# Optimization experiments

Measured on AMD Instinct MI355X. Metric: run time of the kernel, lower is better.

## Reference

```python
import jax, jax.numpy as jnp
import numpy as np

SEQ, BATCH, HIDDEN, HEADS = 2048, 2, 1024, 16
HEAD_DIM = HIDDEN // HEADS
NORM = float(np.sqrt(HEAD_DIM))
NEG_MIN = float(np.finfo(np.float32).min)


def setup_inputs() -> dict:
    key = jax.random.key(0)
    ks = jax.random.split(key, 9)
    xavier = lambda k: (jax.random.normal(k, (HIDDEN, HIDDEN), jnp.float32)
                        * np.sqrt(2.0 / (HIDDEN + HIDDEN)))
    hidden_states = jax.random.normal(ks[0], (SEQ, BATCH, HIDDEN), jnp.float32)
    # causal (left-to-right) bool mask, True = attend
    attention_mask = jnp.tril(jnp.ones((SEQ, SEQ), dtype=bool))[None, None, :, :]
    return {
        "hidden_states": hidden_states,
        "attention_mask": attention_mask,
        "Wq": xavier(ks[1]), "bq": jnp.zeros((HIDDEN,), jnp.float32),
        "Wk": xavier(ks[2]), "bk": jnp.zeros((HIDDEN,), jnp.float32),
        "Wv": xavier(ks[3]), "bv": jnp.zeros((HIDDEN,), jnp.float32),
        "Wo": xavier(ks[4]), "bo": jnp.zeros((HIDDEN,), jnp.float32),
    }


def reference(hidden_states, attention_mask, Wq, bq, Wk, bk, Wv, bv, Wo, bo):
    s, b, _ = hidden_states.shape
    # projections (F.linear: x @ W.T + b), seq-first layout -> [s,b,h,d]
    q = (hidden_states @ Wq.T + bq).reshape(s, b, HEADS, HEAD_DIM) / NORM
    k = (hidden_states @ Wk.T + bk).reshape(s, b, HEADS, HEAD_DIM)
    v = (hidden_states @ Wv.T + bv).reshape(s, b, HEADS, HEAD_DIM)
    # scores [b,h,q,k] (Q already pre-scaled by 1/sqrt(d))
    scores = jnp.einsum("qbhd,kbhd->bhqk", q, k)
    scores = jnp.where(attention_mask, scores, NEG_MIN)
    probs = jax.nn.softmax(scores, axis=-1)
    # context [b,h,q,d] -> permute(2,0,1,3) -> [q,b,h,d] -> [q,b,hidden]
    ctx = jnp.einsum("bhqk,kbhd->qbhd", probs, v).reshape(s, b, HIDDEN)
    return ctx @ Wo.T + bo
```

## Files before the change

### kernel.cpp

```cpp
#include <hip/hip_runtime.h>
#include <hip/hip_bf16.h>
#include <cstdint>
#include <math.h>

#define SEQ 2048
#define BATCH 2
#define HID 1024
#define NH 16
#define HD 64
#define MROWS (SEQ * BATCH)

typedef __attribute__((ext_vector_type(8))) short bf16x8;
typedef __attribute__((ext_vector_type(4))) float f32x4;

typedef const __attribute__((address_space(1))) void* gas_t;
typedef __attribute__((address_space(3))) void* las_t;

static __device__ __forceinline__ unsigned short f2bf(float x) {
    __hip_bfloat16 h = __float2bfloat16(x);
    unsigned short u;
    __builtin_memcpy(&u, &h, 2);
    return u;
}

__global__ __launch_bounds__(256) void f2bf_kern(const float* __restrict__ in,
                                                 unsigned short* __restrict__ out,
                                                 int n8) {
    int i = blockIdx.x * 256 + threadIdx.x;
    if (i >= n8) return;
    const float4* p = (const float4*)in + (size_t)i * 2;
    float4 a = p[0], b = p[1];
    union { unsigned short us[8]; uint4 v; } o;
    o.us[0] = f2bf(a.x); o.us[1] = f2bf(a.y); o.us[2] = f2bf(a.z); o.us[3] = f2bf(a.w);
    o.us[4] = f2bf(b.x); o.us[5] = f2bf(b.y); o.us[6] = f2bf(b.z); o.us[7] = f2bf(b.w);
    ((uint4*)out)[i] = o.v;
}

#define GBK 32

__global__ __launch_bounds__(256, 4) void gemm_bf16(
    const unsigned short* __restrict__ A, const unsigned short* __restrict__ W,
    const float* __restrict__ b0, const float* __restrict__ b1,
    const float* __restrict__ b2,
    unsigned short* __restrict__ Qo, unsigned short* __restrict__ Ko,
    unsigned short* __restrict__ Vo, float* __restrict__ Fo, int mode) {
    __shared__ unsigned short As[2][64 * GBK];
    __shared__ unsigned short Bs[2][128 * GBK];
    const int t = threadIdx.x;
    const int lane = t & 63, w = t >> 6;
    const int wr = w & 1, wc = w >> 1;
    const int m0 = blockIdx.x * 64, n0 = blockIdx.y * 128;

    f32x4 acc[2][4];
#pragma unroll
    for (int i = 0; i < 2; ++i)
#pragma unroll
        for (int j = 0; j < 4; ++j) acc[i][j] = {0.f, 0.f, 0.f, 0.f};

    const int srow = w * 16 + (lane >> 2);
    const int scol = (lane & 3) * 8;
    const unsigned short* gA = A + (size_t)(m0 + srow) * HID + scol;
    const unsigned short* gB = W + (size_t)(n0 + srow) * HID + scol;

    auto stage = [&](int buf, int k0) {
        __builtin_amdgcn_global_load_lds((gas_t)(gA + k0),
                                         (las_t)(&As[buf][(w * 16) * GBK]), 16, 0, 0);
#pragma unroll
        for (int c = 0; c < 2; ++c)
            __builtin_amdgcn_global_load_lds((gas_t)(gB + (size_t)c * 64 * HID + k0),
                                             (las_t)(&Bs[buf][(c * 64 + w * 16) * GBK]), 16, 0, 0);
    };

    const int arow = wr * 32 + (lane & 15);
    const int brow = wc * 64 + (lane & 15);
    const int kfo = (lane >> 4) * 8;

    stage(0, 0);
    int cur = 0;
    for (int k0 = 0; k0 < HID; k0 += GBK) {
        __syncthreads();
        if (k0 + GBK < HID) stage(cur ^ 1, k0 + GBK);
        bf16x8 af[2], bfr[4];
#pragma unroll
        for (int mt = 0; mt < 2; ++mt)
            af[mt] = *(const bf16x8*)(&As[cur][(arow + mt * 16) * GBK + kfo]);
#pragma unroll
        for (int nt = 0; nt < 4; ++nt)
            bfr[nt] = *(const bf16x8*)(&Bs[cur][(brow + nt * 16) * GBK + kfo]);
#pragma unroll
        for (int mt = 0; mt < 2; ++mt)
#pragma unroll
            for (int nt = 0; nt < 4; ++nt)
                acc[mt][nt] = __builtin_amdgcn_mfma_f32_16x16x32_bf16(
                    af[mt], bfr[nt], acc[mt][nt], 0, 0, 0);
        cur ^= 1;
    }

    const int seg = n0 >> 10;
    const float* bias = (mode == 1) ? b0 : (seg == 0 ? b0 : (seg == 1 ? b1 : b2));
    const float scale = (mode == 0 && seg == 0) ? 0.125f : 1.0f;
    const int nbase = (n0 & 1023) + wc * 64;

    float bvals[4];
#pragma unroll
    for (int nt = 0; nt < 4; ++nt)
        bvals[nt] = bias[nbase + nt * 16 + (lane & 15)];

#pragma unroll
    for (int mt = 0; mt < 2; ++mt)
#pragma unroll
        for (int nt = 0; nt < 4; ++nt)
#pragma unroll
            for (int i = 0; i < 4; ++i) {
                float v = (acc[mt][nt][i] + bvals[nt]) * scale;
                int m = m0 + wr * 32 + mt * 16 + (lane >> 4) * 4 + i;
                int n = nbase + nt * 16 + (lane & 15);
                if (mode == 1) {
                    Fo[(size_t)m * HID + n] = v;
                } else if (seg == 0) {
                    Qo[(size_t)m * HID + n] = f2bf(v);
                } else if (seg == 1) {
                    Ko[(size_t)m * HID + n] = f2bf(v);
                } else {
                    Vo[(size_t)n * MROWS + (m & 1) * SEQ + (m >> 1)] = f2bf(v);
                }
            }
}

__global__ __launch_bounds__(256) void attn_mfma(const unsigned short* __restrict__ Qb,
                                                 const unsigned short* __restrict__ Kb,
                                                 const unsigned short* __restrict__ Vt,
                                                 unsigned short* __restrict__ Ob) {
    __shared__ unsigned short Kl[2][64 * 64];
    __shared__ unsigned short Vl[2][64 * 64];
    __shared__ unsigned short QP[64 * 64];

    const int t = threadIdx.x;
    const int lane = t & 63, w = t >> 6;

    const int flat = (int)blockIdx.x + (int)blockIdx.y * 16;
    const int xcd = flat & 7, ii = flat >> 3;
    const int bh = xcd * 4 + (ii >> 4);
    const int p = ii & 15;
    const int b = bh >> 4, h = bh & 15;

    const int lrow_base = w * 8 + (lane >> 3);
    const int chunkb = (lane & 7) * 16;

    for (int pass = 0; pass < 2; ++pass) {
        const int qt = pass == 0 ? (31 - p) : p;
        const int q0 = qt * 64;
        if (pass) __syncthreads();

        auto stage_kv = [&](int buf, int kt) {
            const int k0 = kt * 64;
#pragma unroll
            for (int c = 0; c < 2; ++c) {
                int lr = c * 32 + lrow_base;
                int sb = chunkb ^ ((lr & 7) << 4);
                const unsigned short* ksrc =
                    Kb + ((size_t)(k0 + lr) * 2 + b) * HID + h * 64 + (sb >> 1);
                const unsigned short* vsrc =
                    Vt + (size_t)(h * 64 + lr) * MROWS + b * SEQ + k0 + (sb >> 1);
                __builtin_amdgcn_global_load_lds((gas_t)ksrc,
                    (las_t)(&Kl[buf][(c * 32 + w * 8) * 64]), 16, 0, 0);
                __builtin_amdgcn_global_load_lds((gas_t)vsrc,
                    (las_t)(&Vl[buf][(c * 32 + w * 8) * 64]), 16, 0, 0);
            }
        };

        stage_kv(0, 0);

#pragma unroll
        for (int c = 0; c < 2; ++c) {
            int f = c * 256 + t;
            int r = f >> 3, dc = f & 7;
            uint4 v = *(const uint4*)(Qb + (size_t)((q0 + r) * 2 + b) * HID + h * 64 + dc * 8);
            *(uint4*)((char*)QP + r * 128 + ((dc * 16) ^ ((r & 7) << 4))) = v;
        }

        f32x4 acc[4];
#pragma unroll
        for (int nt = 0; nt < 4; ++nt) acc[nt] = {0.f, 0.f, 0.f, 0.f};
        float mrow[4] = {-INFINITY, -INFINITY, -INFINITY, -INFINITY};
        float lrow[4] = {0.f, 0.f, 0.f, 0.f};
        bf16x8 qf[2];

        int cur = 0;
        for (int kt = 0; kt <= qt; ++kt) {
            __syncthreads();
            if (kt < qt) stage_kv(cur ^ 1, kt + 1);
            if (kt == 0) {
                int r = w * 16 + (lane & 15);
                int base = r * 128, sw = (r & 7) << 4;
                qf[0] = *(const bf16x8*)((char*)QP + base + ((((lane >> 4) * 16) + 0) ^ sw));
                qf[1] = *(const bf16x8*)((char*)QP + base + ((((lane >> 4) * 16) + 64) ^ sw));
            }
            const char* Kc = (const char*)Kl[cur];
            const char* Vc = (const char*)Vl[cur];

            f32x4 s[4];
#pragma unroll
            for (int ct = 0; ct < 4; ++ct) {
                int j = ct * 16 + (lane & 15);
                int base = j * 128, sw = (j & 7) << 4;
                bf16x8 kf0 = *(const bf16x8*)(Kc + base + ((((lane >> 4) * 16) + 0) ^ sw));
                bf16x8 kf1 = *(const bf16x8*)(Kc + base + ((((lane >> 4) * 16) + 64) ^ sw));
                f32x4 z = {0.f, 0.f, 0.f, 0.f};
                z = __builtin_amdgcn_mfma_f32_16x16x32_bf16(qf[0], kf0, z, 0, 0, 0);
                z = __builtin_amdgcn_mfma_f32_16x16x32_bf16(qf[1], kf1, z, 0, 0, 0);
                s[ct] = z;
            }

            if (kt == qt) {
#pragma unroll
                for (int ct = 0; ct < 4; ++ct) {
                    int j = ct * 16 + (lane & 15);
#pragma unroll
                    for (int i = 0; i < 4; ++i) {
                        int q = w * 16 + (lane >> 4) * 4 + i;
                        if (j > q) s[ct][i] = -3.0e38f;
                    }
                }
            }

#pragma unroll
            for (int i = 0; i < 4; ++i) {
                float mx = fmaxf(fmaxf(s[0][i], s[1][i]), fmaxf(s[2][i], s[3][i]));
                mx = fmaxf(mx, __shfl_xor(mx, 1));
                mx = fmaxf(mx, __shfl_xor(mx, 2));
                mx = fmaxf(mx, __shfl_xor(mx, 4));
                mx = fmaxf(mx, __shfl_xor(mx, 8));
                float mn = fmaxf(mrow[i], mx);
                float corr = __expf(mrow[i] - mn);
                mrow[i] = mn;
                float rs = 0.f;
#pragma unroll
                for (int ct = 0; ct < 4; ++ct) {
                    float pe = __expf(s[ct][i] - mn);
                    s[ct][i] = pe;
                    rs += pe;
                }
                rs += __shfl_xor(rs, 1);
                rs += __shfl_xor(rs, 2);
                rs += __shfl_xor(rs, 4);
                rs += __shfl_xor(rs, 8);
                lrow[i] = lrow[i] * corr + rs;
#pragma unroll
                for (int nt = 0; nt < 4; ++nt) acc[nt][i] *= corr;
            }

#pragma unroll
            for (int ct = 0; ct < 4; ++ct)
#pragma unroll
                for (int i = 0; i < 4; ++i) {
                    int r = w * 16 + (lane >> 4) * 4 + i;
                    int jb = (ct * 16 + (lane & 15)) * 2;
                    *(unsigned short*)((char*)QP + r * 128 + (jb ^ ((r & 7) << 4))) = f2bf(s[ct][i]);
                }
            asm volatile("s_waitcnt lgkmcnt(0)" ::: "memory");
            __builtin_amdgcn_sched_barrier(0);

            bf16x8 pf[2];
            {
                int r = w * 16 + (lane & 15);
                int base = r * 128, sw = (r & 7) << 4;
                pf[0] = *(const bf16x8*)((char*)QP + base + ((((lane >> 4) * 16) + 0) ^ sw));
                pf[1] = *(const bf16x8*)((char*)QP + base + ((((lane >> 4) * 16) + 64) ^ sw));
            }
#pragma unroll
            for (int nt = 0; nt < 4; ++nt) {
                int d = nt * 16 + (lane & 15);
                int base = d * 128, sw = (d & 7) << 4;
                bf16x8 v0 = *(const bf16x8*)(Vc + base + ((((lane >> 4) * 16) + 0) ^ sw));
                bf16x8 v1 = *(const bf16x8*)(Vc + base + ((((lane >> 4) * 16) + 64) ^ sw));
                acc[nt] = __builtin_amdgcn_mfma_f32_16x16x32_bf16(pf[0], v0, acc[nt], 0, 0, 0);
                acc[nt] = __builtin_amdgcn_mfma_f32_16x16x32_bf16(pf[1], v1, acc[nt], 0, 0, 0);
            }
            cur ^= 1;
        }

#pragma unroll
        for (int i = 0; i < 4; ++i) {
            float inv = 1.0f / lrow[i];
            int q = q0 + w * 16 + (lane >> 4) * 4 + i;
#pragma unroll
            for (int nt = 0; nt < 4; ++nt) {
                int col = h * 64 + nt * 16 + (lane & 15);
                Ob[(size_t)(q * 2 + b) * HID + col] = f2bf(acc[nt][i] * inv);
            }
        }
    }
}

extern "C" void kernel_launch(void* const* d_in, const int* in_sizes, int n_in,
                              void* d_out, int out_size, void* d_ws, size_t ws_size,
                              hipStream_t stream) {
    const float* hs = (const float*)d_in[0];
    const float* Wq = (const float*)d_in[2];
    const float* bq = (const float*)d_in[3];
    const float* Wk = (const float*)d_in[4];
    const float* bk = (const float*)d_in[5];
    const float* Wv = (const float*)d_in[6];
    const float* bv = (const float*)d_in[7];
    const float* Wo = (const float*)d_in[8];
    const float* bo = (const float*)d_in[9];

    char* ws = (char*)d_ws;
    unsigned short* hs_bf   = (unsigned short*)(ws);
    unsigned short* Wqkv_bf = (unsigned short*)(ws + (8u << 20));
    unsigned short* Wo_bf   = (unsigned short*)(ws + (14u << 20));
    unsigned short* Q_bf    = (unsigned short*)(ws + (16u << 20));
    unsigned short* K_bf    = (unsigned short*)(ws + (24u << 20));
    unsigned short* Vt_bf   = (unsigned short*)(ws + (32u << 20));
    unsigned short* ctx_bf  = (unsigned short*)(ws + (40u << 20));

    dim3 blk(256);
    const int WN8 = HID * HID / 8;
    hipLaunchKernelGGL(f2bf_kern, dim3(MROWS * HID / 8 / 256), blk, 0, stream, hs, hs_bf, MROWS * HID / 8);
    hipLaunchKernelGGL(f2bf_kern, dim3(WN8 / 256), blk, 0, stream, Wq, Wqkv_bf, WN8);
    hipLaunchKernelGGL(f2bf_kern, dim3(WN8 / 256), blk, 0, stream, Wk, Wqkv_bf + (size_t)HID * HID, WN8);
    hipLaunchKernelGGL(f2bf_kern, dim3(WN8 / 256), blk, 0, stream, Wv, Wqkv_bf + (size_t)2 * HID * HID, WN8);
    hipLaunchKernelGGL(f2bf_kern, dim3(WN8 / 256), blk, 0, stream, Wo, Wo_bf, WN8);

    hipLaunchKernelGGL(gemm_bf16, dim3(MROWS / 64, 24), blk, 0, stream,
                       hs_bf, Wqkv_bf, bq, bk, bv, Q_bf, K_bf, Vt_bf, (float*)nullptr, 0);

    hipLaunchKernelGGL(attn_mfma, dim3(16, 32), blk, 0, stream,
                       Q_bf, K_bf, Vt_bf, ctx_bf);

    hipLaunchKernelGGL(gemm_bf16, dim3(MROWS / 64, 8), blk, 0, stream,
                       ctx_bf, Wo_bf, bo, bo, bo,
                       (unsigned short*)nullptr, (unsigned short*)nullptr,
                       (unsigned short*)nullptr, (float*)d_out, 1);
}
```

Measured before the change: 245.7 us.

## Enlarge GEMM tiles via template and give each attention block one query tile

The GEMM becomes a template with 128-row M tiles and a variable N tile: 128 columns for the QKV projection and 64 for the output projection. This raises register reuse per block while keeping the output-projection grid large enough. The attention kernel no longer pairs a long and a short query tile in two passes. It launches one block per query tile (32x32 grid), longest tiles first, spreading causal work across more blocks at the cost of losing the explicit load pairing. The GEMM also drops its occupancy hint of 4 blocks, which may change register allocation.

```diff
diff --git a/kernel.cpp b/kernel.cpp
--- a/kernel.cpp
+++ b/kernel.cpp
@@ -38,41 +38,43 @@
 
 #define GBK 32
 
-__global__ __launch_bounds__(256, 4) void gemm_bf16(
+template <int BNT2>
+__global__ __launch_bounds__(256) void gemm_bf16(
     const unsigned short* __restrict__ A, const unsigned short* __restrict__ W,
     const float* __restrict__ b0, const float* __restrict__ b1,
     const float* __restrict__ b2,
     unsigned short* __restrict__ Qo, unsigned short* __restrict__ Ko,
     unsigned short* __restrict__ Vo, float* __restrict__ Fo, int mode) {
-    __shared__ unsigned short As[2][64 * GBK];
-    __shared__ unsigned short Bs[2][128 * GBK];
+    constexpr int BN = BNT2 * 32;
+    __shared__ unsigned short As[2][128 * GBK];
+    __shared__ unsigned short Bs[2][BN * GBK];
     const int t = threadIdx.x;
     const int lane = t & 63, w = t >> 6;
     const int wr = w & 1, wc = w >> 1;
-    const int m0 = blockIdx.x * 64, n0 = blockIdx.y * 128;
-
-    f32x4 acc[2][4];
-#pragma unroll
-    for (int i = 0; i < 2; ++i)
-#pragma unroll
-        for (int j = 0; j < 4; ++j) acc[i][j] = {0.f, 0.f, 0.f, 0.f};
-
-    const int srow = w * 16 + (lane >> 2);
-    const int scol = (lane & 3) * 8;
-    const unsigned short* gA = A + (size_t)(m0 + srow) * HID + scol;
-    const unsigned short* gB = W + (size_t)(n0 + srow) * HID + scol;
+    const int m0 = blockIdx.x * 128, n0 = blockIdx.y * BN;
+
+    f32x4 acc[4][BNT2];
+#pragma unroll
+    for (int i = 0; i < 4; ++i)
+#pragma unroll
+        for (int j = 0; j < BNT2; ++j) acc[i][j] = {0.f, 0.f, 0.f, 0.f};
+
+    const unsigned short* gA = A + (size_t)(m0 + w * 16 + (lane >> 2)) * HID + (lane & 3) * 8;
+    const unsigned short* gB = W + (size_t)(n0 + w * 16 + (lane >> 2)) * HID + (lane & 3) * 8;
 
     auto stage = [&](int buf, int k0) {
-        __builtin_amdgcn_global_load_lds((gas_t)(gA + k0),
-                                         (las_t)(&As[buf][(w * 16) * GBK]), 16, 0, 0);
 #pragma unroll
         for (int c = 0; c < 2; ++c)
+            __builtin_amdgcn_global_load_lds((gas_t)(gA + (size_t)c * 64 * HID + k0),
+                                             (las_t)(&As[buf][(c * 64 + w * 16) * GBK]), 16, 0, 0);
+#pragma unroll
+        for (int c = 0; c < BN / 64; ++c)
             __builtin_amdgcn_global_load_lds((gas_t)(gB + (size_t)c * 64 * HID + k0),
                                              (las_t)(&Bs[buf][(c * 64 + w * 16) * GBK]), 16, 0, 0);
     };
 
-    const int arow = wr * 32 + (lane & 15);
-    const int brow = wc * 64 + (lane & 15);
+    const int arow = wr * 64 + (lane & 15);
+    const int brow = wc * (BNT2 * 16) + (lane & 15);
     const int kfo = (lane >> 4) * 8;
 
     stage(0, 0);
@@ -80,17 +82,17 @@
     for (int k0 = 0; k0 < HID; k0 += GBK) {
         __syncthreads();
         if (k0 + GBK < HID) stage(cur ^ 1, k0 + GBK);
-        bf16x8 af[2], bfr[4];
-#pragma unroll
-        for (int mt = 0; mt < 2; ++mt)
+        bf16x8 af[4], bfr[BNT2];
+#pragma unroll
+        for (int mt = 0; mt < 4; ++mt)
             af[mt] = *(const bf16x8*)(&As[cur][(arow + mt * 16) * GBK + kfo]);
 #pragma unroll
-        for (int nt = 0; nt < 4; ++nt)
+        for (int nt = 0; nt < BNT2; ++nt)
             bfr[nt] = *(const bf16x8*)(&Bs[cur][(brow + nt * 16) * GBK + kfo]);
 #pragma unroll
-        for (int mt = 0; mt < 2; ++mt)
-#pragma unroll
-            for (int nt = 0; nt < 4; ++nt)
+        for (int mt = 0; mt < 4; ++mt)
+#pragma unroll
+            for (int nt = 0; nt < BNT2; ++nt)
                 acc[mt][nt] = __builtin_amdgcn_mfma_f32_16x16x32_bf16(
                     af[mt], bfr[nt], acc[mt][nt], 0, 0, 0);
         cur ^= 1;
@@ -99,21 +101,21 @@
     const int seg = n0 >> 10;
     const float* bias = (mode == 1) ? b0 : (seg == 0 ? b0 : (seg == 1 ? b1 : b2));
     const float scale = (mode == 0 && seg == 0) ? 0.125f : 1.0f;
-    const int nbase = (n0 & 1023) + wc * 64;
-
-    float bvals[4];
-#pragma unroll
-    for (int nt = 0; nt < 4; ++nt)
+    const int nbase = (n0 & 1023) + wc * (BNT2 * 16);
+
+    float bvals[BNT2];
+#pragma unroll
+    for (int nt = 0; nt < BNT2; ++nt)
         bvals[nt] = bias[nbase + nt * 16 + (lane & 15)];
 
 #pragma unroll
-    for (int mt = 0; mt < 2; ++mt)
-#pragma unroll
-        for (int nt = 0; nt < 4; ++nt)
+    for (int mt = 0; mt < 4; ++mt)
+#pragma unroll
+        for (int nt = 0; nt < BNT2; ++nt)
 #pragma unroll
             for (int i = 0; i < 4; ++i) {
                 float v = (acc[mt][nt][i] + bvals[nt]) * scale;
-                int m = m0 + wr * 32 + mt * 16 + (lane >> 4) * 4 + i;
+                int m = m0 + wr * 64 + mt * 16 + (lane >> 4) * 4 + i;
                 int n = nbase + nt * 16 + (lane & 15);
                 if (mode == 1) {
                     Fo[(size_t)m * HID + n] = v;
@@ -138,157 +140,152 @@
     const int t = threadIdx.x;
     const int lane = t & 63, w = t >> 6;
 
-    const int flat = (int)blockIdx.x + (int)blockIdx.y * 16;
+    const int flat = (int)blockIdx.x + (int)blockIdx.y * 32;
     const int xcd = flat & 7, ii = flat >> 3;
-    const int bh = xcd * 4 + (ii >> 4);
-    const int p = ii & 15;
+    const int bh = xcd * 4 + (ii >> 5);
+    const int qt = 31 - (ii & 31);
     const int b = bh >> 4, h = bh & 15;
+    const int q0 = qt * 64;
 
     const int lrow_base = w * 8 + (lane >> 3);
     const int chunkb = (lane & 7) * 16;
 
-    for (int pass = 0; pass < 2; ++pass) {
-        const int qt = pass == 0 ? (31 - p) : p;
-        const int q0 = qt * 64;
-        if (pass) __syncthreads();
-
-        auto stage_kv = [&](int buf, int kt) {
-            const int k0 = kt * 64;
-#pragma unroll
-            for (int c = 0; c < 2; ++c) {
-                int lr = c * 32 + lrow_base;
-                int sb = chunkb ^ ((lr & 7) << 4);
-                const unsigned short* ksrc =
-                    Kb + ((size_t)(k0 + lr) * 2 + b) * HID + h * 64 + (sb >> 1);
-                const unsigned short* vsrc =
-                    Vt + (size_t)(h * 64 + lr) * MROWS + b * SEQ + k0 + (sb >> 1);
-                __builtin_amdgcn_global_load_lds((gas_t)ksrc,
-                    (las_t)(&Kl[buf][(c * 32 + w * 8) * 64]), 16, 0, 0);
-                __builtin_amdgcn_global_load_lds((gas_t)vsrc,
-                    (las_t)(&Vl[buf][(c * 32 + w * 8) * 64]), 16, 0, 0);
-            }
-        };
-
-        stage_kv(0, 0);
-
+    auto stage_kv = [&](int buf, int kt) {
+        const int k0 = kt * 64;
 #pragma unroll
         for (int c = 0; c < 2; ++c) {
-            int f = c * 256 + t;
-            int r = f >> 3, dc = f & 7;
-            uint4 v = *(const uint4*)(Qb + (size_t)((q0 + r) * 2 + b) * HID + h * 64 + dc * 8);
-            *(uint4*)((char*)QP + r * 128 + ((dc * 16) ^ ((r & 7) << 4))) = v;
-        }
-
-        f32x4 acc[4];
-#pragma unroll
-        for (int nt = 0; nt < 4; ++nt) acc[nt] = {0.f, 0.f, 0.f, 0.f};
-        float mrow[4] = {-INFINITY, -INFINITY, -INFINITY, -INFINITY};
-        float lrow[4] = {0.f, 0.f, 0.f, 0.f};
-        bf16x8 qf[2];
-
-        int cur = 0;
-        for (int kt = 0; kt <= qt; ++kt) {
-            __syncthreads();
-            if (kt < qt) stage_kv(cur ^ 1, kt + 1);
-            if (kt == 0) {
-                int r = w * 16 + (lane & 15);
-                int base = r * 128, sw = (r & 7) << 4;
-                qf[0] = *(const bf16x8*)((char*)QP + base + ((((lane >> 4) * 16) + 0) ^ sw));
-                qf[1] = *(const bf16x8*)((char*)QP + base + ((((lane >> 4) * 16) + 64) ^ sw));
-            }
-            const char* Kc = (const char*)Kl[cur];
-            const char* Vc = (const char*)Vl[cur];
-
-            f32x4 s[4];
+            int lr = c * 32 + lrow_base;
+            int sb = chunkb ^ ((lr & 7) << 4);
+            const unsigned short* ksrc =
+                Kb + ((size_t)(k0 + lr) * 2 + b) * HID + h * 64 + (sb >> 1);
+            const unsigned short* vsrc =
+                Vt + (size_t)(h * 64 + lr) * MROWS + b * SEQ + k0 + (sb >> 1);
+            __builtin_amdgcn_global_load_lds((gas_t)ksrc,
+                (las_t)(&Kl[buf][(c * 32 + w * 8) * 64]), 16, 0, 0);
+            __builtin_amdgcn_global_load_lds((gas_t)vsrc,
+                (las_t)(&Vl[buf][(c * 32 + w * 8) * 64]), 16, 0, 0);
+        }
+    };
+
+    stage_kv(0, 0);
+
+#pragma unroll
+    for (int c = 0; c < 2; ++c) {
+        int f = c * 256 + t;
+        int r = f >> 3, dc = f & 7;
+        uint4 v = *(const uint4*)(Qb + (size_t)((q0 + r) * 2 + b) * HID + h * 64 + dc * 8);
+        *(uint4*)((char*)QP + r * 128 + ((dc * 16) ^ ((r & 7) << 4))) = v;
+    }
+
+    f32x4 acc[4];
+#pragma unroll
+    for (int nt = 0; nt < 4; ++nt) acc[nt] = {0.f, 0.f, 0.f, 0.f};
+    float mrow[4] = {-INFINITY, -INFINITY, -INFINITY, -INFINITY};
+    float lrow[4] = {0.f, 0.f, 0.f, 0.f};
+    bf16x8 qf[2];
+
+    int cur = 0;
+    for (int kt = 0; kt <= qt; ++kt) {
+        __syncthreads();
+        if (kt < qt) stage_kv(cur ^ 1, kt + 1);
+        if (kt == 0) {
+            int r = w * 16 + (lane & 15);
+            int base = r * 128, sw = (r & 7) << 4;
+            qf[0] = *(const bf16x8*)((char*)QP + base + ((((lane >> 4) * 16) + 0) ^ sw));
+            qf[1] = *(const bf16x8*)((char*)QP + base + ((((lane >> 4) * 16) + 64) ^ sw));
+        }
+        const char* Kc = (const char*)Kl[cur];
+        const char* Vc = (const char*)Vl[cur];
+
+        f32x4 s[4];
+#pragma unroll
+        for (int ct = 0; ct < 4; ++ct) {
+            int j = ct * 16 + (lane & 15);
+            int base = j * 128, sw = (j & 7) << 4;
+            bf16x8 kf0 = *(const bf16x8*)(Kc + base + ((((lane >> 4) * 16) + 0) ^ sw));
+            bf16x8 kf1 = *(const bf16x8*)(Kc + base + ((((lane >> 4) * 16) + 64) ^ sw));
+            f32x4 z = {0.f, 0.f, 0.f, 0.f};
+            z = __builtin_amdgcn_mfma_f32_16x16x32_bf16(qf[0], kf0, z, 0, 0, 0);
+            z = __builtin_amdgcn_mfma_f32_16x16x32_bf16(qf[1], kf1, z, 0, 0, 0);
+            s[ct] = z;
+        }
+
+        if (kt == qt) {
 #pragma unroll
             for (int ct = 0; ct < 4; ++ct) {
                 int j = ct * 16 + (lane & 15);
-                int base = j * 128, sw = (j & 7) << 4;
-                bf16x8 kf0 = *(const bf16x8*)(Kc + base + ((((lane >> 4) * 16) + 0) ^ sw));
-                bf16x8 kf1 = *(const bf16x8*)(Kc + base + ((((lane >> 4) * 16) + 64) ^ sw));
-                f32x4 z = {0.f, 0.f, 0.f, 0.f};
-                z = __builtin_amdgcn_mfma_f32_16x16x32_bf16(qf[0], kf0, z, 0, 0, 0);
-                z = __builtin_amdgcn_mfma_f32_16x16x32_bf16(qf[1], kf1, z, 0, 0, 0);
-                s[ct] = z;
-            }
-
-            if (kt == qt) {
-#pragma unroll
-                for (int ct = 0; ct < 4; ++ct) {
-                    int j = ct * 16 + (lane & 15);
-#pragma unroll
-                    for (int i = 0; i < 4; ++i) {
-                        int q = w * 16 + (lane >> 4) * 4 + i;
-                        if (j > q) s[ct][i] = -3.0e38f;
-                    }
+#pragma unroll
+                for (int i = 0; i < 4; ++i) {
+                    int q = w * 16 + (lane >> 4) * 4 + i;
+                    if (j > q) s[ct][i] = -3.0e38f;
                 }
             }
-
+        }
+
+#pragma unroll
+        for (int i = 0; i < 4; ++i) {
+            float mx = fmaxf(fmaxf(s[0][i], s[1][i]), fmaxf(s[2][i], s[3][i]));
+            mx = fmaxf(mx, __shfl_xor(mx, 1));
+            mx = fmaxf(mx, __shfl_xor(mx, 2));
+            mx = fmaxf(mx, __shfl_xor(mx, 4));
+            mx = fmaxf(mx, __shfl_xor(mx, 8));
+            float mn = fmaxf(mrow[i], mx);
+            float corr = __expf(mrow[i] - mn);
+            mrow[i] = mn;
+            float rs = 0.f;
+#pragma unroll
+            for (int ct = 0; ct < 4; ++ct) {
+                float pe = __expf(s[ct][i] - mn);
+                s[ct][i] = pe;
+                rs += pe;
+            }
+            rs += __shfl_xor(rs, 1);
+            rs += __shfl_xor(rs, 2);
+            rs += __shfl_xor(rs, 4);
+            rs += __shfl_xor(rs, 8);
+            lrow[i] = lrow[i] * corr + rs;
+#pragma unroll
+            for (int nt = 0; nt < 4; ++nt) acc[nt][i] *= corr;
+        }
+
+#pragma unroll
+        for (int ct = 0; ct < 4; ++ct)
 #pragma unroll
             for (int i = 0; i < 4; ++i) {
-                float mx = fmaxf(fmaxf(s[0][i], s[1][i]), fmaxf(s[2][i], s[3][i]));
-                mx = fmaxf(mx, __shfl_xor(mx, 1));
-                mx = fmaxf(mx, __shfl_xor(mx, 2));
-                mx = fmaxf(mx, __shfl_xor(mx, 4));
-                mx = fmaxf(mx, __shfl_xor(mx, 8));
-                float mn = fmaxf(mrow[i], mx);
-                float corr = __expf(mrow[i] - mn);
-                mrow[i] = mn;
-                float rs = 0.f;
-#pragma unroll
-                for (int ct = 0; ct < 4; ++ct) {
-                    float pe = __expf(s[ct][i] - mn);
-                    s[ct][i] = pe;
-                    rs += pe;
-                }
-                rs += __shfl_xor(rs, 1);
-                rs += __shfl_xor(rs, 2);
-                rs += __shfl_xor(rs, 4);
-                rs += __shfl_xor(rs, 8);
-                lrow[i] = lrow[i] * corr + rs;
-#pragma unroll
-                for (int nt = 0; nt < 4; ++nt) acc[nt][i] *= corr;
+                int r = w * 16 + (lane >> 4) * 4 + i;
+                int jb = (ct * 16 + (lane & 15)) * 2;
+                *(unsigned short*)((char*)QP + r * 128 + (jb ^ ((r & 7) << 4))) = f2bf(s[ct][i]);
             }
-
-#pragma unroll
-            for (int ct = 0; ct < 4; ++ct)
-#pragma unroll
-                for (int i = 0; i < 4; ++i) {
-                    int r = w * 16 + (lane >> 4) * 4 + i;
-                    int jb = (ct * 16 + (lane & 15)) * 2;
-                    *(unsigned short*)((char*)QP + r * 128 + (jb ^ ((r & 7) << 4))) = f2bf(s[ct][i]);
-                }
-            asm volatile("s_waitcnt lgkmcnt(0)" ::: "memory");
-            __builtin_amdgcn_sched_barrier(0);
-
-            bf16x8 pf[2];
-            {
-                int r = w * 16 + (lane & 15);
-                int base = r * 128, sw = (r & 7) << 4;
-                pf[0] = *(const bf16x8*)((char*)QP + base + ((((lane >> 4) * 16) + 0) ^ sw));
-                pf[1] = *(const bf16x8*)((char*)QP + base + ((((lane >> 4) * 16) + 64) ^ sw));
-            }
-#pragma unroll
-            for (int nt = 0; nt < 4; ++nt) {
-                int d = nt * 16 + (lane & 15);
-                int base = d * 128, sw = (d & 7) << 4;
-                bf16x8 v0 = *(const bf16x8*)(Vc + base + ((((lane >> 4) * 16) + 0) ^ sw));
-                bf16x8 v1 = *(const bf16x8*)(Vc + base + ((((lane >> 4) * 16) + 64) ^ sw));
-                acc[nt] = __builtin_amdgcn_mfma_f32_16x16x32_bf16(pf[0], v0, acc[nt], 0, 0, 0);
-                acc[nt] = __builtin_amdgcn_mfma_f32_16x16x32_bf16(pf[1], v1, acc[nt], 0, 0, 0);
-            }
-            cur ^= 1;
-        }
-
-#pragma unroll
-        for (int i = 0; i < 4; ++i) {
-            float inv = 1.0f / lrow[i];
-            int q = q0 + w * 16 + (lane >> 4) * 4 + i;
-#pragma unroll
-            for (int nt = 0; nt < 4; ++nt) {
-                int col = h * 64 + nt * 16 + (lane & 15);
-                Ob[(size_t)(q * 2 + b) * HID + col] = f2bf(acc[nt][i] * inv);
-            }
+        asm volatile("s_waitcnt lgkmcnt(0)" ::: "memory");
+        __builtin_amdgcn_sched_barrier(0);
+
+        bf16x8 pf[2];
+        {
+            int r = w * 16 + (lane & 15);
+            int base = r * 128, sw = (r & 7) << 4;
+            pf[0] = *(const bf16x8*)((char*)QP + base + ((((lane >> 4) * 16) + 0) ^ sw));
+            pf[1] = *(const bf16x8*)((char*)QP + base + ((((lane >> 4) * 16) + 64) ^ sw));
+        }
+#pragma unroll
+        for (int nt = 0; nt < 4; ++nt) {
+            int d = nt * 16 + (lane & 15);
+            int base = d * 128, sw = (d & 7) << 4;
+            bf16x8 v0 = *(const bf16x8*)(Vc + base + ((((lane >> 4) * 16) + 0) ^ sw));
+            bf16x8 v1 = *(const bf16x8*)(Vc + base + ((((lane >> 4) * 16) + 64) ^ sw));
+            acc[nt] = __builtin_amdgcn_mfma_f32_16x16x32_bf16(pf[0], v0, acc[nt], 0, 0, 0);
+            acc[nt] = __builtin_amdgcn_mfma_f32_16x16x32_bf16(pf[1], v1, acc[nt], 0, 0, 0);
+        }
+        cur ^= 1;
+    }
+
+#pragma unroll
+    for (int i = 0; i < 4; ++i) {
+        float inv = 1.0f / lrow[i];
+        int q = q0 + w * 16 + (lane >> 4) * 4 + i;
+#pragma unroll
+        for (int nt = 0; nt < 4; ++nt) {
+            int col = h * 64 + nt * 16 + (lane & 15);
+            Ob[(size_t)(q * 2 + b) * HID + col] = f2bf(acc[nt][i] * inv);
         }
     }
 }
@@ -323,13 +320,13 @@
     hipLaunchKernelGGL(f2bf_kern, dim3(WN8 / 256), blk, 0, stream, Wv, Wqkv_bf + (size_t)2 * HID * HID, WN8);
     hipLaunchKernelGGL(f2bf_kern, dim3(WN8 / 256), blk, 0, stream, Wo, Wo_bf, WN8);
 
-    hipLaunchKernelGGL(gemm_bf16, dim3(MROWS / 64, 24), blk, 0, stream,
+    hipLaunchKernelGGL((gemm_bf16<4>), dim3(MROWS / 128, 24), blk, 0, stream,
                        hs_bf, Wqkv_bf, bq, bk, bv, Q_bf, K_bf, Vt_bf, (float*)nullptr, 0);
 
-    hipLaunchKernelGGL(attn_mfma, dim3(16, 32), blk, 0, stream,
+    hipLaunchKernelGGL(attn_mfma, dim3(32, 32), blk, 0, stream,
                        Q_bf, K_bf, Vt_bf, ctx_bf);
 
-    hipLaunchKernelGGL(gemm_bf16, dim3(MROWS / 64, 8), blk, 0, stream,
+    hipLaunchKernelGGL((gemm_bf16<2>), dim3(MROWS / 128, 16), blk, 0, stream,
                        ctx_bf, Wo_bf, bo, bo, bo,
                        (unsigned short*)nullptr, (unsigned short*)nullptr,
                        (unsigned short*)nullptr, (float*)d_out, 1);
```

After: 274.6 us. 11.8% more time.

## Enlarge GEMM tiles to 256x256 with triple-buffered LDS and XCD-aware block mapping

Applied to the files above, without the earlier changes.

The projection GEMMs now use 512-thread blocks computing 256x256 output tiles (8x4 MFMA tiles per wave) instead of 64x128. LDS staging moves from double to triple buffering, with explicit vmcnt waits and barriers. Block indices are remapped so neighbouring tiles land on the same XCD, which is meant to improve L2 reuse. The larger tiles cut redundant global loads, but the QKV GEMM drops to 192 blocks and the output GEMM to 64 blocks, which may underfill the GPU, and register pressure rises with 32 accumulators per thread.

```diff
diff --git a/kernel.cpp b/kernel.cpp
--- a/kernel.cpp
+++ b/kernel.cpp
@@ -37,63 +37,86 @@
 }
 
 #define GBK 32
-
-__global__ __launch_bounds__(256, 4) void gemm_bf16(
+#define NTT (HID / GBK)
+
+__global__ __launch_bounds__(512) void gemm_bf16(
     const unsigned short* __restrict__ A, const unsigned short* __restrict__ W,
     const float* __restrict__ b0, const float* __restrict__ b1,
     const float* __restrict__ b2,
     unsigned short* __restrict__ Qo, unsigned short* __restrict__ Ko,
     unsigned short* __restrict__ Vo, float* __restrict__ Fo, int mode) {
-    __shared__ unsigned short As[2][64 * GBK];
-    __shared__ unsigned short Bs[2][128 * GBK];
+    __shared__ unsigned short As[3][256 * GBK];
+    __shared__ unsigned short Bs[3][256 * GBK];
     const int t = threadIdx.x;
     const int lane = t & 63, w = t >> 6;
     const int wr = w & 1, wc = w >> 1;
-    const int m0 = blockIdx.x * 64, n0 = blockIdx.y * 128;
-
-    f32x4 acc[2][4];
-#pragma unroll
-    for (int i = 0; i < 2; ++i)
+
+    const int d = (int)blockIdx.x;
+    const int xcd = d & 7, s = d >> 3;
+    int bx, by;
+    if (mode == 0) {
+        bx = (xcd & 3) * 4 + (s & 3);
+        by = (xcd >> 2) * 6 + (s >> 2);
+    } else {
+        bx = xcd * 2 + (s >> 2);
+        by = s & 3;
+    }
+    const int m0 = bx * 256, n0 = by * 256;
+
+    f32x4 acc[8][4];
+#pragma unroll
+    for (int i = 0; i < 8; ++i)
 #pragma unroll
         for (int j = 0; j < 4; ++j) acc[i][j] = {0.f, 0.f, 0.f, 0.f};
 
-    const int srow = w * 16 + (lane >> 2);
-    const int scol = (lane & 3) * 8;
-    const unsigned short* gA = A + (size_t)(m0 + srow) * HID + scol;
-    const unsigned short* gB = W + (size_t)(n0 + srow) * HID + scol;
-
-    auto stage = [&](int buf, int k0) {
-        __builtin_amdgcn_global_load_lds((gas_t)(gA + k0),
-                                         (las_t)(&As[buf][(w * 16) * GBK]), 16, 0, 0);
-#pragma unroll
-        for (int c = 0; c < 2; ++c)
-            __builtin_amdgcn_global_load_lds((gas_t)(gB + (size_t)c * 64 * HID + k0),
-                                             (las_t)(&Bs[buf][(c * 64 + w * 16) * GBK]), 16, 0, 0);
+    const unsigned short* gA = A + (size_t)(m0 + w * 32 + (lane >> 2)) * HID + (lane & 3) * 8;
+    const unsigned short* gB = W + (size_t)(n0 + w * 32 + (lane >> 2)) * HID + (lane & 3) * 8;
+
+    auto stage = [&](int buf, int kt) {
+        const int k0 = kt * GBK;
+#pragma unroll
+        for (int c = 0; c < 2; ++c) {
+            __builtin_amdgcn_global_load_lds((gas_t)(gA + (size_t)c * 16 * HID + k0),
+                                             (las_t)(&As[buf][(w * 32 + c * 16) * GBK]), 16, 0, 0);
+            __builtin_amdgcn_global_load_lds((gas_t)(gB + (size_t)c * 16 * HID + k0),
+                                             (las_t)(&Bs[buf][(w * 32 + c * 16) * GBK]), 16, 0, 0);
+        }
     };
 
-    const int arow = wr * 32 + (lane & 15);
+    const int arow = wr * 128 + (lane & 15);
     const int brow = wc * 64 + (lane & 15);
     const int kfo = (lane >> 4) * 8;
 
-    stage(0, 0);
-    int cur = 0;
-    for (int k0 = 0; k0 < HID; k0 += GBK) {
-        __syncthreads();
-        if (k0 + GBK < HID) stage(cur ^ 1, k0 + GBK);
-        bf16x8 af[2], bfr[4];
-#pragma unroll
-        for (int mt = 0; mt < 2; ++mt)
-            af[mt] = *(const bf16x8*)(&As[cur][(arow + mt * 16) * GBK + kfo]);
+    stage(0, 0); stage(1, 1); stage(2, 2);
+    int bn = 0;
+    for (int kt = 0; kt < NTT; ++kt) {
+        if (kt <= NTT - 3)
+            asm volatile("s_waitcnt vmcnt(8)" ::: "memory");
+        else if (kt == NTT - 2)
+            asm volatile("s_waitcnt vmcnt(4)" ::: "memory");
+        else
+            asm volatile("s_waitcnt vmcnt(0)" ::: "memory");
+        __builtin_amdgcn_s_barrier();
+
+        bf16x8 af[8], bfr[4];
+#pragma unroll
+        for (int mt = 0; mt < 8; ++mt)
+            af[mt] = *(const bf16x8*)(&As[bn][(arow + mt * 16) * GBK + kfo]);
 #pragma unroll
         for (int nt = 0; nt < 4; ++nt)
-            bfr[nt] = *(const bf16x8*)(&Bs[cur][(brow + nt * 16) * GBK + kfo]);
-#pragma unroll
-        for (int mt = 0; mt < 2; ++mt)
+            bfr[nt] = *(const bf16x8*)(&Bs[bn][(brow + nt * 16) * GBK + kfo]);
+#pragma unroll
+        for (int mt = 0; mt < 8; ++mt)
 #pragma unroll
             for (int nt = 0; nt < 4; ++nt)
                 acc[mt][nt] = __builtin_amdgcn_mfma_f32_16x16x32_bf16(
                     af[mt], bfr[nt], acc[mt][nt], 0, 0, 0);
-        cur ^= 1;
+
+        asm volatile("s_waitcnt lgkmcnt(0)" ::: "memory");
+        __builtin_amdgcn_sched_barrier(0);
+        __builtin_amdgcn_s_barrier();
+        if (kt + 3 < NTT) stage(bn, kt + 3);
+        bn = (bn == 2) ? 0 : bn + 1;
     }
 
     const int seg = n0 >> 10;
@@ -107,13 +130,13 @@
         bvals[nt] = bias[nbase + nt * 16 + (lane & 15)];
 
 #pragma unroll
-    for (int mt = 0; mt < 2; ++mt)
+    for (int mt = 0; mt < 8; ++mt)
 #pragma unroll
         for (int nt = 0; nt < 4; ++nt)
 #pragma unroll
             for (int i = 0; i < 4; ++i) {
                 float v = (acc[mt][nt][i] + bvals[nt]) * scale;
-                int m = m0 + wr * 32 + mt * 16 + (lane >> 4) * 4 + i;
+                int m = m0 + wr * 128 + mt * 16 + (lane >> 4) * 4 + i;
                 int n = nbase + nt * 16 + (lane & 15);
                 if (mode == 1) {
                     Fo[(size_t)m * HID + n] = v;
@@ -270,8 +293,8 @@
             }
 #pragma unroll
             for (int nt = 0; nt < 4; ++nt) {
-                int d = nt * 16 + (lane & 15);
-                int base = d * 128, sw = (d & 7) << 4;
+                int dd = nt * 16 + (lane & 15);
+                int base = dd * 128, sw = (dd & 7) << 4;
                 bf16x8 v0 = *(const bf16x8*)(Vc + base + ((((lane >> 4) * 16) + 0) ^ sw));
                 bf16x8 v1 = *(const bf16x8*)(Vc + base + ((((lane >> 4) * 16) + 64) ^ sw));
                 acc[nt] = __builtin_amdgcn_mfma_f32_16x16x32_bf16(pf[0], v0, acc[nt], 0, 0, 0);
@@ -315,7 +338,7 @@
     unsigned short* Vt_bf   = (unsigned short*)(ws + (32u << 20));
     unsigned short* ctx_bf  = (unsigned short*)(ws + (40u << 20));
 
-    dim3 blk(256);
+    dim3 blk(256), blk2(512);
     const int WN8 = HID * HID / 8;
     hipLaunchKernelGGL(f2bf_kern, dim3(MROWS * HID / 8 / 256), blk, 0, stream, hs, hs_bf, MROWS * HID / 8);
     hipLaunchKernelGGL(f2bf_kern, dim3(WN8 / 256), blk, 0, stream, Wq, Wqkv_bf, WN8);
@@ -323,13 +346,13 @@
     hipLaunchKernelGGL(f2bf_kern, dim3(WN8 / 256), blk, 0, stream, Wv, Wqkv_bf + (size_t)2 * HID * HID, WN8);
     hipLaunchKernelGGL(f2bf_kern, dim3(WN8 / 256), blk, 0, stream, Wo, Wo_bf, WN8);
 
-    hipLaunchKernelGGL(gemm_bf16, dim3(MROWS / 64, 24), blk, 0, stream,
+    hipLaunchKernelGGL(gemm_bf16, dim3(192), blk2, 0, stream,
                        hs_bf, Wqkv_bf, bq, bk, bv, Q_bf, K_bf, Vt_bf, (float*)nullptr, 0);
 
     hipLaunchKernelGGL(attn_mfma, dim3(16, 32), blk, 0, stream,
                        Q_bf, K_bf, Vt_bf, ctx_bf);
 
-    hipLaunchKernelGGL(gemm_bf16, dim3(MROWS / 64, 8), blk, 0, stream,
+    hipLaunchKernelGGL(gemm_bf16, dim3(64), blk2, 0, stream,
                        ctx_bf, Wo_bf, bo, bo, bo,
                        (unsigned short*)nullptr, (unsigned short*)nullptr,
                        (unsigned short*)nullptr, (float*)d_out, 1);
```

Result: slower. 290.6 us (+18.2%).
